# Kernel optimization log

Measured on AMD Instinct MI355X. Metric: run time of the kernel, lower is better.

Reference implementation:

```python
import jax, jax.numpy as jnp
import numpy as np

B, LQ, LK, H, A = 32, 2048, 2048, 1024, 512


def setup_inputs() -> dict:
    key = jax.random.key(0)
    ks = jax.random.split(key, 5)
    s = 1.0 / np.sqrt(H)
    return {
        "query": jax.random.normal(ks[0], (B, LQ, H), jnp.float32),
        "key": jax.random.normal(ks[1], (B, LK, H), jnp.float32),
        "Wq": jax.random.normal(ks[2], (H, A), jnp.float32) * s,
        "bq": jnp.zeros((A,), jnp.float32),
        "Wk": jax.random.normal(ks[3], (H, A), jnp.float32) * s,
        "bk": jnp.zeros((A,), jnp.float32),
        "Wv": jax.random.normal(ks[4], (A, 1), jnp.float32) * (1.0 / np.sqrt(A)),
        "bv": jnp.zeros((1,), jnp.float32),
    }


def reference(query, key, Wq, bq, Wk, bk, Wv, bv):
    # Linear projections
    Qp = jnp.einsum("bqh,ha->bqa", query, Wq) + bq          # [B, LQ, A]
    Kp = jnp.einsum("bkh,ha->bka", key, Wk) + bk            # [B, LK, A]
    # Score matrix Q(query) @ K(key)^T
    alpha_mat = jnp.einsum("bqa,bka->bqk", Qp, Kp)          # [B, LQ, LK]
    # Sum over query dim, softmax over key dim
    alpha = jax.nn.softmax(alpha_mat.sum(axis=1, keepdims=True), axis=2)  # [B, 1, LK]
    # Per-key scalar head V applied to projected keys, then weighted combine
    v = jnp.einsum("bka,ao->bko", Kp, Wv) + bv              # [B, LK, 1]
    x = jnp.matmul(alpha, v)[:, 0, :]                        # [B, 1]
    return x
```

## Files before the change

### kernel.cpp

```cpp
#include <hip/hip_runtime.h>
#include <math.h>

#define NB 32
#define LQ 2048
#define LK 2048
#define HD 1024
#define AD 512
#define QCH 32

__global__ void __launch_bounds__(256) k1_qreduce(const float* __restrict__ query,
                                                 const float* __restrict__ Wk,
                                                 const float* __restrict__ Wv,
                                                 const float* __restrict__ bk,
                                                 const float* __restrict__ bv,
                                                 float* __restrict__ partial,
                                                 float* __restrict__ wv_eff,
                                                 float* __restrict__ c_v) {
    int bid = blockIdx.x;
    if (bid < NB * QCH) {
        int b = bid / QCH, qc = bid % QCH;
        int t = threadIdx.x;
        const int QPC = LQ / QCH;
        float4 a0 = {0.f, 0.f, 0.f, 0.f};
        float4 a1 = {0.f, 0.f, 0.f, 0.f};
        const float4* src = (const float4*)(query + ((size_t)b * LQ + (size_t)qc * QPC) * HD);
        for (int q = 0; q < QPC; q += 2) {
            float4 v0 = src[(size_t)q * (HD / 4) + t];
            float4 v1 = src[(size_t)(q + 1) * (HD / 4) + t];
            a0.x += v0.x; a0.y += v0.y; a0.z += v0.z; a0.w += v0.w;
            a1.x += v1.x; a1.y += v1.y; a1.z += v1.z; a1.w += v1.w;
        }
        float4 acc = {a0.x + a1.x, a0.y + a1.y, a0.z + a1.z, a0.w + a1.w};
        float4* dst = (float4*)(partial + ((size_t)qc * NB + b) * HD);
        dst[t] = acc;
    } else if (bid < NB * QCH + 16) {
        int w = threadIdx.x >> 6, lane = threadIdx.x & 63;
        int gw = (bid - NB * QCH) * 4 + w;
        const float4* vv = (const float4*)(Wv);
        for (int r = 0; r < 16; ++r) {
            int h = gw * 16 + r;
            const float4* wr = (const float4*)(Wk + (size_t)h * AD);
            double acc = 0.0;
            #pragma unroll
            for (int j = 0; j < 2; ++j) {
                int f = lane + 64 * j;
                float4 w4 = wr[f];
                float4 v4 = vv[f];
                acc += (double)w4.x * (double)v4.x + (double)w4.y * (double)v4.y
                     + (double)w4.z * (double)v4.z + (double)w4.w * (double)v4.w;
            }
            #pragma unroll
            for (int off = 32; off > 0; off >>= 1) acc += __shfl_down(acc, off);
            if (lane == 0) wv_eff[h] = (float)acc;
        }
    } else {
        if (threadIdx.x < 64) {
            int lane = threadIdx.x;
            const float4* br = (const float4*)(bk);
            const float4* vv = (const float4*)(Wv);
            double acc = 0.0;
            #pragma unroll
            for (int j = 0; j < 2; ++j) {
                int f = lane + 64 * j;
                float4 b4 = br[f];
                float4 v4 = vv[f];
                acc += (double)b4.x * (double)v4.x + (double)b4.y * (double)v4.y
                     + (double)b4.z * (double)v4.z + (double)b4.w * (double)v4.w;
            }
            #pragma unroll
            for (int off = 32; off > 0; off >>= 1) acc += __shfl_down(acc, off);
            if (lane == 0) c_v[0] = (float)(acc + (double)bv[0]);
        }
    }
}

__global__ void __launch_bounds__(256) kB_qsum(const float* __restrict__ partial,
                                               const float* __restrict__ Wq,
                                               const float* __restrict__ bq,
                                               float* __restrict__ qsum) {
    __shared__ float sq[HD];
    __shared__ double red[4][64];
    int b = blockIdx.x >> 3;
    int a0 = (blockIdx.x & 7) * 64;
    int t = threadIdx.x;

    #pragma unroll
    for (int c = 0; c < 4; ++c) {
        int h = t + c * 256;
        float acc = 0.f;
        #pragma unroll 4
        for (int qc = 0; qc < QCH; ++qc)
            acc += partial[((size_t)qc * NB + b) * HD + h];
        sq[h] = acc;
    }
    __syncthreads();

    int w = t >> 6, lane = t & 63;
    int a = a0 + lane;
    const float* wp = Wq + a;
    double c0 = 0.0, c1 = 0.0, c2 = 0.0, c3 = 0.0;
    int hbase = w * 256;
    for (int i = 0; i < 256; i += 4) {
        int h = hbase + i;
        c0 += (double)sq[h]     * (double)wp[(size_t)h * AD];
        c1 += (double)sq[h + 1] * (double)wp[(size_t)(h + 1) * AD];
        c2 += (double)sq[h + 2] * (double)wp[(size_t)(h + 2) * AD];
        c3 += (double)sq[h + 3] * (double)wp[(size_t)(h + 3) * AD];
    }
    red[w][lane] = ((c0 + c1) + (c2 + c3));
    __syncthreads();
    if (t < 64) {
        double s = red[0][t] + red[1][t] + red[2][t] + red[3][t];
        qsum[(size_t)b * AD + a0 + t] = (float)(s + (double)LQ * (double)bq[a0 + t]);
    }
}

__global__ void __launch_bounds__(256) k4_weff(const float* __restrict__ qsum,
                                               const float* __restrict__ Wk,
                                               float* __restrict__ wk_eff) {
    int w = threadIdx.x >> 6, lane = threadIdx.x & 63;
    int widx = blockIdx.x * 4 + w;
    int b = widx >> 10, h = widx & (HD - 1);
    const float4* wr = (const float4*)(Wk + (size_t)h * AD);
    const float4* qs = (const float4*)(qsum + (size_t)b * AD);
    double acc = 0.0;
    #pragma unroll
    for (int j = 0; j < 2; ++j) {
        int f = lane + 64 * j;
        float4 w4 = wr[f];
        float4 q4 = qs[f];
        acc += (double)w4.x * (double)q4.x + (double)w4.y * (double)q4.y
             + (double)w4.z * (double)q4.z + (double)w4.w * (double)q4.w;
    }
    #pragma unroll
    for (int off = 32; off > 0; off >>= 1) acc += __shfl_down(acc, off);
    if (lane == 0) wk_eff[widx] = (float)acc;
}

__global__ void __launch_bounds__(256) k5_scores(const float* __restrict__ key,
                                                 const float* __restrict__ wk_eff,
                                                 const float* __restrict__ wv_eff,
                                                 const float* __restrict__ c_v,
                                                 float* __restrict__ scores,
                                                 float* __restrict__ vvals) {
    __shared__ float lwk[HD];
    __shared__ float lwv[HD];
    int bid = blockIdx.x;
    int b = bid >> 6;
    int k0 = (bid & 63) * 32;
    for (int i = threadIdx.x; i < HD; i += 256) {
        lwk[i] = wk_eff[(size_t)b * HD + i];
        lwv[i] = wv_eff[i];
    }
    __syncthreads();
    int w = threadIdx.x >> 6;
    int lane = threadIdx.x & 63;
    double cv = (double)c_v[0];
    const float4* lwk4 = (const float4*)lwk;
    const float4* lwv4 = (const float4*)lwv;
    for (int r = 0; r < 8; ++r) {
        int k = k0 + w * 8 + r;
        const float4* kr = (const float4*)(key + ((size_t)b * LK + k) * HD);
        double sc = 0.0, vv = 0.0;
        #pragma unroll
        for (int j = 0; j < 4; ++j) {
            int f = lane + 64 * j;
            float4 kv  = kr[f];
            float4 wk4 = lwk4[f];
            float4 wv4 = lwv4[f];
            sc += (double)kv.x * (double)wk4.x + (double)kv.y * (double)wk4.y
                + (double)kv.z * (double)wk4.z + (double)kv.w * (double)wk4.w;
            vv += (double)kv.x * (double)wv4.x + (double)kv.y * (double)wv4.y
                + (double)kv.z * (double)wv4.z + (double)kv.w * (double)wv4.w;
        }
        #pragma unroll
        for (int off = 32; off > 0; off >>= 1) {
            sc += __shfl_down(sc, off);
            vv += __shfl_down(vv, off);
        }
        if (lane == 0) {
            scores[(size_t)b * LK + k] = (float)sc;
            vvals[(size_t)b * LK + k]  = (float)(vv + cv);
        }
    }
}

__global__ void __launch_bounds__(256) k6_softmax(const float* __restrict__ scores,
                                                  const float* __restrict__ vvals,
                                                  float* __restrict__ out) {
    int b = blockIdx.x;
    int t = threadIdx.x;
    __shared__ float smax_sh[4];
    __shared__ double num_sh[4], den_sh[4];
    const float* sr = scores + (size_t)b * LK;
    const float* vr = vvals  + (size_t)b * LK;
    float m = -INFINITY;
    for (int k = t; k < LK; k += 256) m = fmaxf(m, sr[k]);
    #pragma unroll
    for (int off = 32; off > 0; off >>= 1) m = fmaxf(m, __shfl_down(m, off));
    int w = t >> 6, lane = t & 63;
    if (lane == 0) smax_sh[w] = m;
    __syncthreads();
    float gm = fmaxf(fmaxf(smax_sh[0], smax_sh[1]), fmaxf(smax_sh[2], smax_sh[3]));
    double num = 0.0, den = 0.0;
    for (int k = t; k < LK; k += 256) {
        double e = exp((double)(sr[k] - gm));
        den += e;
        num += e * (double)vr[k];
    }
    #pragma unroll
    for (int off = 32; off > 0; off >>= 1) {
        num += __shfl_down(num, off);
        den += __shfl_down(den, off);
    }
    if (lane == 0) { num_sh[w] = num; den_sh[w] = den; }
    __syncthreads();
    if (t == 0) {
        double N = num_sh[0] + num_sh[1] + num_sh[2] + num_sh[3];
        double D = den_sh[0] + den_sh[1] + den_sh[2] + den_sh[3];
        out[b] = (float)(N / D);
    }
}

extern "C" void kernel_launch(void* const* d_in, const int* in_sizes, int n_in,
                              void* d_out, int out_size, void* d_ws, size_t ws_size,
                              hipStream_t stream) {
    const float* query = (const float*)d_in[0];
    const float* key   = (const float*)d_in[1];
    const float* Wq    = (const float*)d_in[2];
    const float* bq    = (const float*)d_in[3];
    const float* Wk    = (const float*)d_in[4];
    const float* bk    = (const float*)d_in[5];
    const float* Wv    = (const float*)d_in[6];
    const float* bv    = (const float*)d_in[7];
    float* out = (float*)d_out;

    float* ws = (float*)d_ws;
    size_t off = 0;
    float* partial = ws + off; off += (size_t)QCH * NB * HD;
    float* qsum    = ws + off; off += (size_t)NB * AD;
    float* wk_eff  = ws + off; off += (size_t)NB * HD;
    float* wv_eff  = ws + off; off += (size_t)HD;
    float* c_v     = ws + off; off += 1;
    float* scores  = ws + off; off += (size_t)NB * LK;
    float* vvals   = ws + off; off += (size_t)NB * LK;

    hipLaunchKernelGGL(k1_qreduce, dim3(NB * QCH + 16 + 1), dim3(256), 0, stream,
                       query, Wk, Wv, bk, bv, partial, wv_eff, c_v);
    hipLaunchKernelGGL(kB_qsum, dim3(NB * 8), dim3(256), 0, stream, partial, Wq, bq, qsum);
    hipLaunchKernelGGL(k4_weff, dim3(NB * HD / 4), dim3(256), 0, stream, qsum, Wk, wk_eff);
    hipLaunchKernelGGL(k5_scores, dim3(NB * (LK / 32)), dim3(256), 0, stream,
                       key, wk_eff, wv_eff, c_v, scores, vvals);
    hipLaunchKernelGGL(k6_softmax, dim3(NB), dim3(256), 0, stream, scores, vvals, out);
}
```

Measured before the change: 148.6 us.

## Fuse all phases into one cooperative persistent kernel with grid syncs

Merges the five separate kernels into a single cooperative kernel that runs the phases in sequence, separated by grid-wide barriers, on a persistent grid sized by occupancy. It also regroups the work per block: phase 4 handles two key rows per iteration and phase 3 handles eight rows per wave. The goal is to remove per-kernel launch gaps and tail effects, at the cost of grid.sync overhead and a grid limited to resident blocks. A fallback path launches the phases as separate kernels if the cooperative launch fails.

```diff
diff --git a/kernel.cpp b/kernel.cpp
--- a/kernel.cpp
+++ b/kernel.cpp
@@ -1,5 +1,8 @@
 #include <hip/hip_runtime.h>
+#include <hip/hip_cooperative_groups.h>
 #include <math.h>
+
+namespace cg = cooperative_groups;
 
 #define NB 32
 #define LQ 2048
@@ -8,18 +11,10 @@
 #define AD 512
 #define QCH 32
 
-__global__ void __launch_bounds__(256) k1_qreduce(const float* __restrict__ query,
-                                                 const float* __restrict__ Wk,
-                                                 const float* __restrict__ Wv,
-                                                 const float* __restrict__ bk,
-                                                 const float* __restrict__ bv,
-                                                 float* __restrict__ partial,
-                                                 float* __restrict__ wv_eff,
-                                                 float* __restrict__ c_v) {
-    int bid = blockIdx.x;
-    if (bid < NB * QCH) {
-        int b = bid / QCH, qc = bid % QCH;
-        int t = threadIdx.x;
+__device__ __forceinline__ void phase1(int G, int bid, int t,
+        const float* __restrict__ query, float* __restrict__ partial) {
+    for (int task = bid; task < NB * QCH; task += G) {
+        int b = task / QCH, qc = task % QCH;
         const int QPC = LQ / QCH;
         float4 a0 = {0.f, 0.f, 0.f, 0.f};
         float4 a1 = {0.f, 0.f, 0.f, 0.f};
@@ -31,15 +26,55 @@
             a1.x += v1.x; a1.y += v1.y; a1.z += v1.z; a1.w += v1.w;
         }
         float4 acc = {a0.x + a1.x, a0.y + a1.y, a0.z + a1.z, a0.w + a1.w};
-        float4* dst = (float4*)(partial + ((size_t)qc * NB + b) * HD);
-        dst[t] = acc;
-    } else if (bid < NB * QCH + 16) {
-        int w = threadIdx.x >> 6, lane = threadIdx.x & 63;
-        int gw = (bid - NB * QCH) * 4 + w;
-        const float4* vv = (const float4*)(Wv);
-        for (int r = 0; r < 16; ++r) {
-            int h = gw * 16 + r;
+        ((float4*)(partial + ((size_t)qc * NB + b) * HD))[t] = acc;
+    }
+}
+
+__device__ __forceinline__ void phase2(int G, int bid, int t,
+        const float* __restrict__ partial, const float* __restrict__ Wq,
+        const float* __restrict__ bq, const float* __restrict__ Wk,
+        const float* __restrict__ Wv, const float* __restrict__ bk,
+        const float* __restrict__ bv, float* __restrict__ qsum,
+        float* __restrict__ wv_eff, float* __restrict__ c_v) {
+    __shared__ float sq[HD];
+    __shared__ double red[4][64];
+    int w = t >> 6, lane = t & 63;
+    for (int task = bid; task < 513; task += G) {
+        if (task < 256) {
+            int b = task >> 3;
+            int a0 = (task & 7) * 64;
+            #pragma unroll
+            for (int c = 0; c < 4; ++c) {
+                int h = t + c * 256;
+                float acc = 0.f;
+                #pragma unroll 4
+                for (int qc = 0; qc < QCH; ++qc)
+                    acc += partial[((size_t)qc * NB + b) * HD + h];
+                sq[h] = acc;
+            }
+            __syncthreads();
+            int a = a0 + lane;
+            const float* wp = Wq + a;
+            double c0 = 0.0, c1 = 0.0, c2 = 0.0, c3 = 0.0;
+            int hbase = w * 256;
+            for (int i = 0; i < 256; i += 4) {
+                int h = hbase + i;
+                c0 += (double)sq[h]     * (double)wp[(size_t)h * AD];
+                c1 += (double)sq[h + 1] * (double)wp[(size_t)(h + 1) * AD];
+                c2 += (double)sq[h + 2] * (double)wp[(size_t)(h + 2) * AD];
+                c3 += (double)sq[h + 3] * (double)wp[(size_t)(h + 3) * AD];
+            }
+            red[w][lane] = ((c0 + c1) + (c2 + c3));
+            __syncthreads();
+            if (t < 64) {
+                double s = red[0][t] + red[1][t] + red[2][t] + red[3][t];
+                qsum[(size_t)b * AD + a0 + t] = (float)(s + (double)LQ * (double)bq[a0 + t]);
+            }
+            __syncthreads();
+        } else if (task < 512) {
+            int h = (task - 256) * 4 + w;
             const float4* wr = (const float4*)(Wk + (size_t)h * AD);
+            const float4* vv = (const float4*)(Wv);
             double acc = 0.0;
             #pragma unroll
             for (int j = 0; j < 2; ++j) {
@@ -52,174 +87,205 @@
             #pragma unroll
             for (int off = 32; off > 0; off >>= 1) acc += __shfl_down(acc, off);
             if (lane == 0) wv_eff[h] = (float)acc;
-        }
-    } else {
-        if (threadIdx.x < 64) {
-            int lane = threadIdx.x;
-            const float4* br = (const float4*)(bk);
-            const float4* vv = (const float4*)(Wv);
+        } else {
+            if (t < 64) {
+                const float4* br = (const float4*)(bk);
+                const float4* vv = (const float4*)(Wv);
+                double acc = 0.0;
+                #pragma unroll
+                for (int j = 0; j < 2; ++j) {
+                    int f = lane + 64 * j;
+                    float4 b4 = br[f];
+                    float4 v4 = vv[f];
+                    acc += (double)b4.x * (double)v4.x + (double)b4.y * (double)v4.y
+                         + (double)b4.z * (double)v4.z + (double)b4.w * (double)v4.w;
+                }
+                #pragma unroll
+                for (int off = 32; off > 0; off >>= 1) acc += __shfl_down(acc, off);
+                if (lane == 0) c_v[0] = (float)(acc + (double)bv[0]);
+            }
+        }
+    }
+}
+
+__device__ __forceinline__ void phase3(int G, int bid, int t,
+        const float* __restrict__ qsum, const float* __restrict__ Wk,
+        float* __restrict__ wk_eff) {
+    int w = t >> 6, lane = t & 63;
+    for (int task = bid; task < 1024; task += G) {
+        int base = task * 32 + w * 8;
+        for (int r = 0; r < 8; ++r) {
+            int idx = base + r;
+            int b = idx >> 10, h = idx & (HD - 1);
+            const float4* wr = (const float4*)(Wk + (size_t)h * AD);
+            const float4* qs = (const float4*)(qsum + (size_t)b * AD);
             double acc = 0.0;
             #pragma unroll
             for (int j = 0; j < 2; ++j) {
                 int f = lane + 64 * j;
-                float4 b4 = br[f];
-                float4 v4 = vv[f];
-                acc += (double)b4.x * (double)v4.x + (double)b4.y * (double)v4.y
-                     + (double)b4.z * (double)v4.z + (double)b4.w * (double)v4.w;
+                float4 w4 = wr[f];
+                float4 q4 = qs[f];
+                acc += (double)w4.x * (double)q4.x + (double)w4.y * (double)q4.y
+                     + (double)w4.z * (double)q4.z + (double)w4.w * (double)q4.w;
             }
             #pragma unroll
             for (int off = 32; off > 0; off >>= 1) acc += __shfl_down(acc, off);
-            if (lane == 0) c_v[0] = (float)(acc + (double)bv[0]);
-        }
-    }
-}
-
-__global__ void __launch_bounds__(256) kB_qsum(const float* __restrict__ partial,
-                                               const float* __restrict__ Wq,
-                                               const float* __restrict__ bq,
-                                               float* __restrict__ qsum) {
-    __shared__ float sq[HD];
-    __shared__ double red[4][64];
-    int b = blockIdx.x >> 3;
-    int a0 = (blockIdx.x & 7) * 64;
-    int t = threadIdx.x;
-
-    #pragma unroll
-    for (int c = 0; c < 4; ++c) {
-        int h = t + c * 256;
-        float acc = 0.f;
-        #pragma unroll 4
-        for (int qc = 0; qc < QCH; ++qc)
-            acc += partial[((size_t)qc * NB + b) * HD + h];
-        sq[h] = acc;
-    }
-    __syncthreads();
-
-    int w = t >> 6, lane = t & 63;
-    int a = a0 + lane;
-    const float* wp = Wq + a;
-    double c0 = 0.0, c1 = 0.0, c2 = 0.0, c3 = 0.0;
-    int hbase = w * 256;
-    for (int i = 0; i < 256; i += 4) {
-        int h = hbase + i;
-        c0 += (double)sq[h]     * (double)wp[(size_t)h * AD];
-        c1 += (double)sq[h + 1] * (double)wp[(size_t)(h + 1) * AD];
-        c2 += (double)sq[h + 2] * (double)wp[(size_t)(h + 2) * AD];
-        c3 += (double)sq[h + 3] * (double)wp[(size_t)(h + 3) * AD];
-    }
-    red[w][lane] = ((c0 + c1) + (c2 + c3));
-    __syncthreads();
-    if (t < 64) {
-        double s = red[0][t] + red[1][t] + red[2][t] + red[3][t];
-        qsum[(size_t)b * AD + a0 + t] = (float)(s + (double)LQ * (double)bq[a0 + t]);
-    }
-}
-
-__global__ void __launch_bounds__(256) k4_weff(const float* __restrict__ qsum,
-                                               const float* __restrict__ Wk,
-                                               float* __restrict__ wk_eff) {
-    int w = threadIdx.x >> 6, lane = threadIdx.x & 63;
-    int widx = blockIdx.x * 4 + w;
-    int b = widx >> 10, h = widx & (HD - 1);
-    const float4* wr = (const float4*)(Wk + (size_t)h * AD);
-    const float4* qs = (const float4*)(qsum + (size_t)b * AD);
-    double acc = 0.0;
-    #pragma unroll
-    for (int j = 0; j < 2; ++j) {
-        int f = lane + 64 * j;
-        float4 w4 = wr[f];
-        float4 q4 = qs[f];
-        acc += (double)w4.x * (double)q4.x + (double)w4.y * (double)q4.y
-             + (double)w4.z * (double)q4.z + (double)w4.w * (double)q4.w;
-    }
-    #pragma unroll
-    for (int off = 32; off > 0; off >>= 1) acc += __shfl_down(acc, off);
-    if (lane == 0) wk_eff[widx] = (float)acc;
-}
-
-__global__ void __launch_bounds__(256) k5_scores(const float* __restrict__ key,
-                                                 const float* __restrict__ wk_eff,
-                                                 const float* __restrict__ wv_eff,
-                                                 const float* __restrict__ c_v,
-                                                 float* __restrict__ scores,
-                                                 float* __restrict__ vvals) {
+            if (lane == 0) wk_eff[idx] = (float)acc;
+        }
+    }
+}
+
+__device__ __forceinline__ void phase4(int G, int bid, int t,
+        const float* __restrict__ key, const float* __restrict__ wk_eff,
+        const float* __restrict__ wv_eff, const float* __restrict__ c_v,
+        float* __restrict__ scores, float* __restrict__ vvals) {
     __shared__ float lwk[HD];
     __shared__ float lwv[HD];
-    int bid = blockIdx.x;
-    int b = bid >> 6;
-    int k0 = (bid & 63) * 32;
-    for (int i = threadIdx.x; i < HD; i += 256) {
-        lwk[i] = wk_eff[(size_t)b * HD + i];
-        lwv[i] = wv_eff[i];
-    }
-    __syncthreads();
-    int w = threadIdx.x >> 6;
-    int lane = threadIdx.x & 63;
-    double cv = (double)c_v[0];
-    const float4* lwk4 = (const float4*)lwk;
-    const float4* lwv4 = (const float4*)lwv;
-    for (int r = 0; r < 8; ++r) {
-        int k = k0 + w * 8 + r;
-        const float4* kr = (const float4*)(key + ((size_t)b * LK + k) * HD);
-        double sc = 0.0, vv = 0.0;
+    int w = t >> 6, lane = t & 63;
+    for (int task = bid; task < 1024; task += G) {
+        int b = task >> 5;
+        int k0 = (task & 31) * 64;
+        for (int i = t; i < HD; i += 256) {
+            lwk[i] = wk_eff[(size_t)b * HD + i];
+            lwv[i] = wv_eff[i];
+        }
+        __syncthreads();
+        double cv = (double)c_v[0];
+        const float4* lwk4 = (const float4*)lwk;
+        const float4* lwv4 = (const float4*)lwv;
+        for (int rp = 0; rp < 8; ++rp) {
+            int k = k0 + w * 16 + rp * 2;
+            const float4* kr0 = (const float4*)(key + ((size_t)b * LK + k) * HD);
+            const float4* kr1 = kr0 + (HD / 4);
+            double sc0 = 0.0, vv0 = 0.0, sc1 = 0.0, vv1 = 0.0;
+            #pragma unroll
+            for (int j = 0; j < 4; ++j) {
+                int f = lane + 64 * j;
+                float4 k0v = kr0[f];
+                float4 k1v = kr1[f];
+                float4 wk4 = lwk4[f];
+                float4 wv4 = lwv4[f];
+                sc0 += (double)k0v.x * (double)wk4.x + (double)k0v.y * (double)wk4.y
+                     + (double)k0v.z * (double)wk4.z + (double)k0v.w * (double)wk4.w;
+                vv0 += (double)k0v.x * (double)wv4.x + (double)k0v.y * (double)wv4.y
+                     + (double)k0v.z * (double)wv4.z + (double)k0v.w * (double)wv4.w;
+                sc1 += (double)k1v.x * (double)wk4.x + (double)k1v.y * (double)wk4.y
+                     + (double)k1v.z * (double)wk4.z + (double)k1v.w * (double)wk4.w;
+                vv1 += (double)k1v.x * (double)wv4.x + (double)k1v.y * (double)wv4.y
+                     + (double)k1v.z * (double)wv4.z + (double)k1v.w * (double)wv4.w;
+            }
+            #pragma unroll
+            for (int off = 32; off > 0; off >>= 1) {
+                sc0 += __shfl_down(sc0, off);
+                vv0 += __shfl_down(vv0, off);
+                sc1 += __shfl_down(sc1, off);
+                vv1 += __shfl_down(vv1, off);
+            }
+            if (lane == 0) {
+                scores[(size_t)b * LK + k]     = (float)sc0;
+                vvals [(size_t)b * LK + k]     = (float)(vv0 + cv);
+                scores[(size_t)b * LK + k + 1] = (float)sc1;
+                vvals [(size_t)b * LK + k + 1] = (float)(vv1 + cv);
+            }
+        }
+        __syncthreads();
+    }
+}
+
+__device__ __forceinline__ void phase5(int G, int bid, int t,
+        const float* __restrict__ scores, const float* __restrict__ vvals,
+        float* __restrict__ out) {
+    __shared__ float smax_sh[4];
+    __shared__ double num_sh[4], den_sh[4];
+    int w = t >> 6, lane = t & 63;
+    for (int b = bid; b < NB; b += G) {
+        const float* sr = scores + (size_t)b * LK;
+        const float* vr = vvals  + (size_t)b * LK;
+        float m = -INFINITY;
+        for (int k = t; k < LK; k += 256) m = fmaxf(m, sr[k]);
         #pragma unroll
-        for (int j = 0; j < 4; ++j) {
-            int f = lane + 64 * j;
-            float4 kv  = kr[f];
-            float4 wk4 = lwk4[f];
-            float4 wv4 = lwv4[f];
-            sc += (double)kv.x * (double)wk4.x + (double)kv.y * (double)wk4.y
-                + (double)kv.z * (double)wk4.z + (double)kv.w * (double)wk4.w;
-            vv += (double)kv.x * (double)wv4.x + (double)kv.y * (double)wv4.y
-                + (double)kv.z * (double)wv4.z + (double)kv.w * (double)wv4.w;
+        for (int off = 32; off > 0; off >>= 1) m = fmaxf(m, __shfl_down(m, off));
+        if (lane == 0) smax_sh[w] = m;
+        __syncthreads();
+        float gm = fmaxf(fmaxf(smax_sh[0], smax_sh[1]), fmaxf(smax_sh[2], smax_sh[3]));
+        double num = 0.0, den = 0.0;
+        for (int k = t; k < LK; k += 256) {
+            double e = exp((double)(sr[k] - gm));
+            den += e;
+            num += e * (double)vr[k];
         }
         #pragma unroll
         for (int off = 32; off > 0; off >>= 1) {
-            sc += __shfl_down(sc, off);
-            vv += __shfl_down(vv, off);
-        }
-        if (lane == 0) {
-            scores[(size_t)b * LK + k] = (float)sc;
-            vvals[(size_t)b * LK + k]  = (float)(vv + cv);
-        }
-    }
-}
-
-__global__ void __launch_bounds__(256) k6_softmax(const float* __restrict__ scores,
-                                                  const float* __restrict__ vvals,
-                                                  float* __restrict__ out) {
-    int b = blockIdx.x;
-    int t = threadIdx.x;
-    __shared__ float smax_sh[4];
-    __shared__ double num_sh[4], den_sh[4];
-    const float* sr = scores + (size_t)b * LK;
-    const float* vr = vvals  + (size_t)b * LK;
-    float m = -INFINITY;
-    for (int k = t; k < LK; k += 256) m = fmaxf(m, sr[k]);
-    #pragma unroll
-    for (int off = 32; off > 0; off >>= 1) m = fmaxf(m, __shfl_down(m, off));
-    int w = t >> 6, lane = t & 63;
-    if (lane == 0) smax_sh[w] = m;
-    __syncthreads();
-    float gm = fmaxf(fmaxf(smax_sh[0], smax_sh[1]), fmaxf(smax_sh[2], smax_sh[3]));
-    double num = 0.0, den = 0.0;
-    for (int k = t; k < LK; k += 256) {
-        double e = exp((double)(sr[k] - gm));
-        den += e;
-        num += e * (double)vr[k];
-    }
-    #pragma unroll
-    for (int off = 32; off > 0; off >>= 1) {
-        num += __shfl_down(num, off);
-        den += __shfl_down(den, off);
-    }
-    if (lane == 0) { num_sh[w] = num; den_sh[w] = den; }
-    __syncthreads();
-    if (t == 0) {
-        double N = num_sh[0] + num_sh[1] + num_sh[2] + num_sh[3];
-        double D = den_sh[0] + den_sh[1] + den_sh[2] + den_sh[3];
-        out[b] = (float)(N / D);
-    }
+            num += __shfl_down(num, off);
+            den += __shfl_down(den, off);
+        }
+        if (lane == 0) { num_sh[w] = num; den_sh[w] = den; }
+        __syncthreads();
+        if (t == 0) {
+            double N = num_sh[0] + num_sh[1] + num_sh[2] + num_sh[3];
+            double D = den_sh[0] + den_sh[1] + den_sh[2] + den_sh[3];
+            out[b] = (float)(N / D);
+        }
+        __syncthreads();
+    }
+}
+
+__global__ void __launch_bounds__(256, 4)
+fused_all(const float* __restrict__ query, const float* __restrict__ key,
+          const float* __restrict__ Wq, const float* __restrict__ bq,
+          const float* __restrict__ Wk, const float* __restrict__ bk,
+          const float* __restrict__ Wv, const float* __restrict__ bv,
+          float* __restrict__ partial, float* __restrict__ qsum,
+          float* __restrict__ wk_eff, float* __restrict__ wv_eff,
+          float* __restrict__ c_v, float* __restrict__ scores,
+          float* __restrict__ vvals, float* __restrict__ out) {
+    cg::grid_group grid = cg::this_grid();
+    const int G = gridDim.x, bid = blockIdx.x, t = threadIdx.x;
+    phase1(G, bid, t, query, partial);
+    grid.sync();
+    phase2(G, bid, t, partial, Wq, bq, Wk, Wv, bk, bv, qsum, wv_eff, c_v);
+    grid.sync();
+    phase3(G, bid, t, qsum, Wk, wk_eff);
+    grid.sync();
+    phase4(G, bid, t, key, wk_eff, wv_eff, c_v, scores, vvals);
+    grid.sync();
+    phase5(G, bid, t, scores, vvals, out);
+}
+
+__global__ void __launch_bounds__(256) kp1(const float* __restrict__ query,
+                                           float* __restrict__ partial) {
+    phase1(gridDim.x, blockIdx.x, threadIdx.x, query, partial);
+}
+__global__ void __launch_bounds__(256) kp2(const float* __restrict__ partial,
+                                           const float* __restrict__ Wq,
+                                           const float* __restrict__ bq,
+                                           const float* __restrict__ Wk,
+                                           const float* __restrict__ Wv,
+                                           const float* __restrict__ bk,
+                                           const float* __restrict__ bv,
+                                           float* __restrict__ qsum,
+                                           float* __restrict__ wv_eff,
+                                           float* __restrict__ c_v) {
+    phase2(gridDim.x, blockIdx.x, threadIdx.x, partial, Wq, bq, Wk, Wv, bk, bv,
+           qsum, wv_eff, c_v);
+}
+__global__ void __launch_bounds__(256) kp3(const float* __restrict__ qsum,
+                                           const float* __restrict__ Wk,
+                                           float* __restrict__ wk_eff) {
+    phase3(gridDim.x, blockIdx.x, threadIdx.x, qsum, Wk, wk_eff);
+}
+__global__ void __launch_bounds__(256) kp4(const float* __restrict__ key,
+                                           const float* __restrict__ wk_eff,
+                                           const float* __restrict__ wv_eff,
+                                           const float* __restrict__ c_v,
+                                           float* __restrict__ scores,
+                                           float* __restrict__ vvals) {
+    phase4(gridDim.x, blockIdx.x, threadIdx.x, key, wk_eff, wv_eff, c_v, scores, vvals);
+}
+__global__ void __launch_bounds__(256) kp5(const float* __restrict__ scores,
+                                           const float* __restrict__ vvals,
+                                           float* __restrict__ out) {
+    phase5(gridDim.x, blockIdx.x, threadIdx.x, scores, vvals, out);
 }
 
 extern "C" void kernel_launch(void* const* d_in, const int* in_sizes, int n_in,
@@ -245,11 +311,37 @@
     float* scores  = ws + off; off += (size_t)NB * LK;
     float* vvals   = ws + off; off += (size_t)NB * LK;
 
-    hipLaunchKernelGGL(k1_qreduce, dim3(NB * QCH + 16 + 1), dim3(256), 0, stream,
-                       query, Wk, Wv, bk, bv, partial, wv_eff, c_v);
-    hipLaunchKernelGGL(kB_qsum, dim3(NB * 8), dim3(256), 0, stream, partial, Wq, bq, qsum);
-    hipLaunchKernelGGL(k4_weff, dim3(NB * HD / 4), dim3(256), 0, stream, qsum, Wk, wk_eff);
-    hipLaunchKernelGGL(k5_scores, dim3(NB * (LK / 32)), dim3(256), 0, stream,
-                       key, wk_eff, wv_eff, c_v, scores, vvals);
-    hipLaunchKernelGGL(k6_softmax, dim3(NB), dim3(256), 0, stream, scores, vvals, out);
-}
+    int dev = 0;
+    (void)hipGetDevice(&dev);
+    int numCU = 0;
+    (void)hipDeviceGetAttribute(&numCU, hipDeviceAttributeMultiprocessorCount, dev);
+    int maxBlk = 0;
+    hipError_t occ = hipOccupancyMaxActiveBlocksPerMultiprocessor(
+        &maxBlk, (const void*)fused_all, 256, 0);
+
+    hipError_t st = hipErrorUnknown;
+    if (occ == hipSuccess && numCU > 0 && maxBlk > 0) {
+        int G = maxBlk * numCU;
+        if (G > NB * QCH) G = NB * QCH;
+        if (G >= 64) {
+            void* args[] = {
+                (void*)&query, (void*)&key, (void*)&Wq, (void*)&bq,
+                (void*)&Wk, (void*)&bk, (void*)&Wv, (void*)&bv,
+                (void*)&partial, (void*)&qsum, (void*)&wk_eff, (void*)&wv_eff,
+                (void*)&c_v, (void*)&scores, (void*)&vvals, (void*)&out
+            };
+            st = hipLaunchCooperativeKernel((const void*)fused_all, dim3(G), dim3(256),
+                                            args, 0, stream);
+        }
+    }
+
+    if (st != hipSuccess) {
+        hipLaunchKernelGGL(kp1, dim3(NB * QCH), dim3(256), 0, stream, query, partial);
+        hipLaunchKernelGGL(kp2, dim3(513), dim3(256), 0, stream,
+                           partial, Wq, bq, Wk, Wv, bk, bv, qsum, wv_eff, c_v);
+        hipLaunchKernelGGL(kp3, dim3(1024), dim3(256), 0, stream, qsum, Wk, wk_eff);
+        hipLaunchKernelGGL(kp4, dim3(1024), dim3(256), 0, stream,
+                           key, wk_eff, wv_eff, c_v, scores, vvals);
+        hipLaunchKernelGGL(kp5, dim3(NB), dim3(256), 0, stream, scores, vvals, out);
+    }
+}
```

Measured after the change: 395.9 us. 2.66x slower.

## Precompute Wk·Wq^T product, merge reduction kernels, fuse softmax via last-block atomic

Applied to the files above, without the earlier changes.

The query-side chain is reassociated. A 1024x1024 matrix MT = Wk·Wq^T is built with an LDS-tiled fp32 GEMM inside the first kernel, alongside the query row-sum blocks. wk_eff is then one matvec of the summed query against MT plus a bias term, which removes the separate qsum and weff kernels. The softmax-weighted combine moves into the score kernel: the last block per batch, found with an atomic counter, does the final reduction. This cuts launches from five to three, but adds a roughly 1G-FLOP weight GEMM per call and a workspace-size fallback path.

```diff
diff --git a/kernel.cpp b/kernel.cpp
--- a/kernel.cpp
+++ b/kernel.cpp
@@ -8,18 +8,21 @@
 #define AD 512
 #define QCH 32
 
-__global__ void __launch_bounds__(256) k1_qreduce(const float* __restrict__ query,
-                                                 const float* __restrict__ Wk,
-                                                 const float* __restrict__ Wv,
-                                                 const float* __restrict__ bk,
-                                                 const float* __restrict__ bv,
-                                                 float* __restrict__ partial,
-                                                 float* __restrict__ wv_eff,
-                                                 float* __restrict__ c_v) {
-    int bid = blockIdx.x;
-    if (bid < NB * QCH) {
-        int b = bid / QCH, qc = bid % QCH;
-        int t = threadIdx.x;
+__global__ void __launch_bounds__(256, 4)
+k1_main(const float* __restrict__ query, const float* __restrict__ Wq,
+        const float* __restrict__ Wk, const float* __restrict__ Wv,
+        const float* __restrict__ bq, const float* __restrict__ bk,
+        const float* __restrict__ bv, float* __restrict__ partial,
+        float* __restrict__ MT, float* __restrict__ wv_eff,
+        float* __restrict__ ck, float* __restrict__ c_v) {
+    __shared__ float wq_l[128][33];
+    __shared__ float wk_l[32][33];
+    const int bid = blockIdx.x;
+    const int t = threadIdx.x;
+
+    if (bid >= 256) {
+        int task = bid - 256;
+        int b = task / QCH, qc = task % QCH;
         const int QPC = LQ / QCH;
         float4 a0 = {0.f, 0.f, 0.f, 0.f};
         float4 a1 = {0.f, 0.f, 0.f, 0.f};
@@ -31,12 +34,251 @@
             a1.x += v1.x; a1.y += v1.y; a1.z += v1.z; a1.w += v1.w;
         }
         float4 acc = {a0.x + a1.x, a0.y + a1.y, a0.z + a1.z, a0.w + a1.w};
-        float4* dst = (float4*)(partial + ((size_t)qc * NB + b) * HD);
-        dst[t] = acc;
+        ((float4*)(partial + ((size_t)qc * NB + b) * HD))[t] = acc;
+        return;
+    }
+
+    const int hb = bid >> 3;
+    const int pb = bid & 7;
+    const int hgrp = t >> 5;
+    const int pgrp = t & 31;
+    float acc[4][4] = {{0.f}};
+    for (int ac = 0; ac < 16; ++ac) {
+        for (int s = t; s < 128 * 32; s += 256) {
+            int row = s >> 5, a = s & 31;
+            wq_l[row][a] = Wq[(size_t)(pb * 128 + row) * AD + ac * 32 + a];
+        }
+        for (int s = t; s < 32 * 32; s += 256) {
+            int row = s >> 5, a = s & 31;
+            wk_l[row][a] = Wk[(size_t)(hb * 32 + row) * AD + ac * 32 + a];
+        }
+        __syncthreads();
+        #pragma unroll 8
+        for (int a = 0; a < 32; ++a) {
+            float k0 = wk_l[hgrp][a],      k1 = wk_l[hgrp + 8][a],
+                  k2 = wk_l[hgrp + 16][a], k3 = wk_l[hgrp + 24][a];
+            float q0 = wq_l[pgrp][a],      q1 = wq_l[pgrp + 32][a],
+                  q2 = wq_l[pgrp + 64][a], q3 = wq_l[pgrp + 96][a];
+            acc[0][0] += k0*q0; acc[0][1] += k0*q1; acc[0][2] += k0*q2; acc[0][3] += k0*q3;
+            acc[1][0] += k1*q0; acc[1][1] += k1*q1; acc[1][2] += k1*q2; acc[1][3] += k1*q3;
+            acc[2][0] += k2*q0; acc[2][1] += k2*q1; acc[2][2] += k2*q2; acc[2][3] += k2*q3;
+            acc[3][0] += k3*q0; acc[3][1] += k3*q1; acc[3][2] += k3*q2; acc[3][3] += k3*q3;
+        }
+        __syncthreads();
+    }
+    #pragma unroll
+    for (int i = 0; i < 4; ++i)
+        #pragma unroll
+        for (int j = 0; j < 4; ++j)
+            MT[(size_t)(hb * 32 + hgrp + 8 * i) * HD + pb * 128 + pgrp + 32 * j] = acc[i][j];
+
+    if (pb == 0) {
+        int w = t >> 6, lane = t & 63;
+        const float4* vv4 = (const float4*)Wv;
+        const float4* bq4 = (const float4*)bq;
+        for (int rr = 0; rr < 8; ++rr) {
+            int h = hb * 32 + w * 8 + rr;
+            const float4* wr = (const float4*)(Wk + (size_t)h * AD);
+            double a1 = 0.0, a2 = 0.0;
+            #pragma unroll
+            for (int j = 0; j < 2; ++j) {
+                int f = lane + 64 * j;
+                float4 w4 = wr[f];
+                float4 v4 = vv4[f];
+                float4 b4 = bq4[f];
+                a1 += (double)w4.x * v4.x + (double)w4.y * v4.y
+                    + (double)w4.z * v4.z + (double)w4.w * v4.w;
+                a2 += (double)b4.x * w4.x + (double)b4.y * w4.y
+                    + (double)b4.z * w4.z + (double)b4.w * w4.w;
+            }
+            #pragma unroll
+            for (int off = 32; off > 0; off >>= 1) {
+                a1 += __shfl_down(a1, off);
+                a2 += __shfl_down(a2, off);
+            }
+            if (lane == 0) {
+                wv_eff[h] = (float)a1;
+                ck[h] = (float)((double)LQ * a2);
+            }
+        }
+    }
+    if (bid == 0 && t < 64) {
+        int lane = t;
+        const float4* br = (const float4*)bk;
+        const float4* vv4 = (const float4*)Wv;
+        double acc2 = 0.0;
+        #pragma unroll
+        for (int j = 0; j < 2; ++j) {
+            int f = lane + 64 * j;
+            float4 b4 = br[f];
+            float4 v4 = vv4[f];
+            acc2 += (double)b4.x * v4.x + (double)b4.y * v4.y
+                  + (double)b4.z * v4.z + (double)b4.w * v4.w;
+        }
+        #pragma unroll
+        for (int off = 32; off > 0; off >>= 1) acc2 += __shfl_down(acc2, off);
+        if (lane == 0) c_v[0] = (float)(acc2 + (double)bv[0]);
+    }
+}
+
+__global__ void __launch_bounds__(256)
+k2_wkeff(const float* __restrict__ partial, const float* __restrict__ MT,
+         const float* __restrict__ ck, float* __restrict__ wk_eff,
+         int* __restrict__ cnt) {
+    __shared__ float sq[HD];
+    const int bid = blockIdx.x;
+    const int t = threadIdx.x;
+    const int b = bid >> 3, hc = bid & 7;
+    if (bid == 0 && t < NB) cnt[t] = 0;
+    for (int h = t; h < HD; h += 256) {
+        float acc = 0.f;
+        #pragma unroll 4
+        for (int qc = 0; qc < QCH; ++qc)
+            acc += partial[((size_t)qc * NB + b) * HD + h];
+        sq[h] = acc;
+    }
+    __syncthreads();
+    int w = t >> 6, lane = t & 63;
+    const float4* sq4 = (const float4*)sq;
+    for (int rr = 0; rr < 32; ++rr) {
+        int h = hc * 128 + w * 32 + rr;
+        const float4* m4 = (const float4*)(MT + (size_t)h * HD);
+        double acc = 0.0;
+        #pragma unroll
+        for (int f0 = 0; f0 < 4; ++f0) {
+            int f = lane + 64 * f0;
+            float4 m = m4[f];
+            float4 s = sq4[f];
+            acc += (double)m.x * s.x + (double)m.y * s.y
+                 + (double)m.z * s.z + (double)m.w * s.w;
+        }
+        #pragma unroll
+        for (int off = 32; off > 0; off >>= 1) acc += __shfl_down(acc, off);
+        if (lane == 0) wk_eff[(size_t)b * HD + h] = (float)(acc + (double)ck[h]);
+    }
+}
+
+__global__ void __launch_bounds__(256)
+k3_scores(const float* __restrict__ key, const float* __restrict__ wk_eff,
+          const float* __restrict__ wv_eff, const float* __restrict__ c_v,
+          float* __restrict__ scores, float* __restrict__ vvals,
+          int* __restrict__ cnt, float* __restrict__ out) {
+    __shared__ float lwk[HD];
+    __shared__ float lwv[HD];
+    __shared__ int lastFlag;
+    __shared__ float smax_sh[4];
+    __shared__ double num_sh[4], den_sh[4];
+    const int bid = blockIdx.x;
+    const int b = bid >> 6;
+    const int k0 = (bid & 63) * 32;
+    const int t = threadIdx.x;
+    for (int i = t; i < HD; i += 256) {
+        lwk[i] = wk_eff[(size_t)b * HD + i];
+        lwv[i] = wv_eff[i];
+    }
+    __syncthreads();
+    int w = t >> 6, lane = t & 63;
+    double cv = (double)c_v[0];
+    const float4* lwk4 = (const float4*)lwk;
+    const float4* lwv4 = (const float4*)lwv;
+    for (int rp = 0; rp < 4; ++rp) {
+        int k = k0 + w * 8 + rp * 2;
+        const float4* kr0 = (const float4*)(key + ((size_t)b * LK + k) * HD);
+        const float4* kr1 = kr0 + (HD / 4);
+        double sc0 = 0.0, vv0 = 0.0, sc1 = 0.0, vv1 = 0.0;
+        #pragma unroll
+        for (int j = 0; j < 4; ++j) {
+            int f = lane + 64 * j;
+            float4 k0v = kr0[f];
+            float4 k1v = kr1[f];
+            float4 wk4 = lwk4[f];
+            float4 wv4 = lwv4[f];
+            sc0 += (double)k0v.x * wk4.x + (double)k0v.y * wk4.y
+                 + (double)k0v.z * wk4.z + (double)k0v.w * wk4.w;
+            vv0 += (double)k0v.x * wv4.x + (double)k0v.y * wv4.y
+                 + (double)k0v.z * wv4.z + (double)k0v.w * wv4.w;
+            sc1 += (double)k1v.x * wk4.x + (double)k1v.y * wk4.y
+                 + (double)k1v.z * wk4.z + (double)k1v.w * wk4.w;
+            vv1 += (double)k1v.x * wv4.x + (double)k1v.y * wv4.y
+                 + (double)k1v.z * wv4.z + (double)k1v.w * wv4.w;
+        }
+        #pragma unroll
+        for (int off = 32; off > 0; off >>= 1) {
+            sc0 += __shfl_down(sc0, off);
+            vv0 += __shfl_down(vv0, off);
+            sc1 += __shfl_down(sc1, off);
+            vv1 += __shfl_down(vv1, off);
+        }
+        if (lane == 0) {
+            scores[(size_t)b * LK + k]     = (float)sc0;
+            vvals [(size_t)b * LK + k]     = (float)(vv0 + cv);
+            scores[(size_t)b * LK + k + 1] = (float)sc1;
+            vvals [(size_t)b * LK + k + 1] = (float)(vv1 + cv);
+        }
+    }
+    __syncthreads();
+    if (t == 0) {
+        __threadfence();
+        int old = atomicAdd(&cnt[b], 1);
+        lastFlag = (old == 63) ? 1 : 0;
+    }
+    __syncthreads();
+    if (!lastFlag) return;
+    __threadfence();
+
+    const float* sr = scores + (size_t)b * LK;
+    const float* vr = vvals  + (size_t)b * LK;
+    float m = -INFINITY;
+    for (int k = t; k < LK; k += 256) m = fmaxf(m, sr[k]);
+    #pragma unroll
+    for (int off = 32; off > 0; off >>= 1) m = fmaxf(m, __shfl_down(m, off));
+    if (lane == 0) smax_sh[w] = m;
+    __syncthreads();
+    float gm = fmaxf(fmaxf(smax_sh[0], smax_sh[1]), fmaxf(smax_sh[2], smax_sh[3]));
+    double num = 0.0, den = 0.0;
+    for (int k = t; k < LK; k += 256) {
+        double e = exp((double)(sr[k] - gm));
+        den += e;
+        num += e * (double)vr[k];
+    }
+    #pragma unroll
+    for (int off = 32; off > 0; off >>= 1) {
+        num += __shfl_down(num, off);
+        den += __shfl_down(den, off);
+    }
+    if (lane == 0) { num_sh[w] = num; den_sh[w] = den; }
+    __syncthreads();
+    if (t == 0) {
+        double N = num_sh[0] + num_sh[1] + num_sh[2] + num_sh[3];
+        double D = den_sh[0] + den_sh[1] + den_sh[2] + den_sh[3];
+        out[b] = (float)(N / D);
+    }
+}
+
+__global__ void __launch_bounds__(256)
+fbA(const float* __restrict__ query, const float* __restrict__ Wk,
+    const float* __restrict__ Wv, const float* __restrict__ bk,
+    const float* __restrict__ bv, float* __restrict__ partial,
+    float* __restrict__ wv_eff, float* __restrict__ c_v) {
+    int bid = blockIdx.x;
+    int t = threadIdx.x;
+    if (bid < NB * QCH) {
+        int b = bid / QCH, qc = bid % QCH;
+        const int QPC = LQ / QCH;
+        float4 a0 = {0.f,0.f,0.f,0.f}, a1 = {0.f,0.f,0.f,0.f};
+        const float4* src = (const float4*)(query + ((size_t)b * LQ + (size_t)qc * QPC) * HD);
+        for (int q = 0; q < QPC; q += 2) {
+            float4 v0 = src[(size_t)q * (HD / 4) + t];
+            float4 v1 = src[(size_t)(q + 1) * (HD / 4) + t];
+            a0.x += v0.x; a0.y += v0.y; a0.z += v0.z; a0.w += v0.w;
+            a1.x += v1.x; a1.y += v1.y; a1.z += v1.z; a1.w += v1.w;
+        }
+        float4 acc = {a0.x + a1.x, a0.y + a1.y, a0.z + a1.z, a0.w + a1.w};
+        ((float4*)(partial + ((size_t)qc * NB + b) * HD))[t] = acc;
     } else if (bid < NB * QCH + 16) {
-        int w = threadIdx.x >> 6, lane = threadIdx.x & 63;
+        int w = t >> 6, lane = t & 63;
         int gw = (bid - NB * QCH) * 4 + w;
-        const float4* vv = (const float4*)(Wv);
+        const float4* vv = (const float4*)Wv;
         for (int r = 0; r < 16; ++r) {
             int h = gw * 16 + r;
             const float4* wr = (const float4*)(Wk + (size_t)h * AD);
@@ -46,44 +288,41 @@
                 int f = lane + 64 * j;
                 float4 w4 = wr[f];
                 float4 v4 = vv[f];
-                acc += (double)w4.x * (double)v4.x + (double)w4.y * (double)v4.y
-                     + (double)w4.z * (double)v4.z + (double)w4.w * (double)v4.w;
+                acc += (double)w4.x * v4.x + (double)w4.y * v4.y
+                     + (double)w4.z * v4.z + (double)w4.w * v4.w;
             }
             #pragma unroll
             for (int off = 32; off > 0; off >>= 1) acc += __shfl_down(acc, off);
             if (lane == 0) wv_eff[h] = (float)acc;
         }
-    } else {
-        if (threadIdx.x < 64) {
-            int lane = threadIdx.x;
-            const float4* br = (const float4*)(bk);
-            const float4* vv = (const float4*)(Wv);
-            double acc = 0.0;
-            #pragma unroll
-            for (int j = 0; j < 2; ++j) {
-                int f = lane + 64 * j;
-                float4 b4 = br[f];
-                float4 v4 = vv[f];
-                acc += (double)b4.x * (double)v4.x + (double)b4.y * (double)v4.y
-                     + (double)b4.z * (double)v4.z + (double)b4.w * (double)v4.w;
-            }
-            #pragma unroll
-            for (int off = 32; off > 0; off >>= 1) acc += __shfl_down(acc, off);
-            if (lane == 0) c_v[0] = (float)(acc + (double)bv[0]);
-        }
-    }
-}
-
-__global__ void __launch_bounds__(256) kB_qsum(const float* __restrict__ partial,
-                                               const float* __restrict__ Wq,
-                                               const float* __restrict__ bq,
-                                               float* __restrict__ qsum) {
+    } else if (t < 64) {
+        int lane = t;
+        const float4* br = (const float4*)bk;
+        const float4* vv = (const float4*)Wv;
+        double acc = 0.0;
+        #pragma unroll
+        for (int j = 0; j < 2; ++j) {
+            int f = lane + 64 * j;
+            float4 b4 = br[f];
+            float4 v4 = vv[f];
+            acc += (double)b4.x * v4.x + (double)b4.y * v4.y
+                 + (double)b4.z * v4.z + (double)b4.w * v4.w;
+        }
+        #pragma unroll
+        for (int off = 32; off > 0; off >>= 1) acc += __shfl_down(acc, off);
+        if (lane == 0) c_v[0] = (float)(acc + (double)bv[0]);
+    }
+}
+
+__global__ void __launch_bounds__(256)
+fbB(const float* __restrict__ partial, const float* __restrict__ Wq,
+    const float* __restrict__ bq, float* __restrict__ qsum, int* __restrict__ cnt) {
     __shared__ float sq[HD];
     __shared__ double red[4][64];
     int b = blockIdx.x >> 3;
     int a0 = (blockIdx.x & 7) * 64;
     int t = threadIdx.x;
-
+    if (blockIdx.x == 0 && t < NB) cnt[t] = 0;
     #pragma unroll
     for (int c = 0; c < 4; ++c) {
         int h = t + c * 256;
@@ -94,7 +333,6 @@
         sq[h] = acc;
     }
     __syncthreads();
-
     int w = t >> 6, lane = t & 63;
     int a = a0 + lane;
     const float* wp = Wq + a;
@@ -102,22 +340,22 @@
     int hbase = w * 256;
     for (int i = 0; i < 256; i += 4) {
         int h = hbase + i;
-        c0 += (double)sq[h]     * (double)wp[(size_t)h * AD];
-        c1 += (double)sq[h + 1] * (double)wp[(size_t)(h + 1) * AD];
-        c2 += (double)sq[h + 2] * (double)wp[(size_t)(h + 2) * AD];
-        c3 += (double)sq[h + 3] * (double)wp[(size_t)(h + 3) * AD];
+        c0 += (double)sq[h]     * wp[(size_t)h * AD];
+        c1 += (double)sq[h + 1] * wp[(size_t)(h + 1) * AD];
+        c2 += (double)sq[h + 2] * wp[(size_t)(h + 2) * AD];
+        c3 += (double)sq[h + 3] * wp[(size_t)(h + 3) * AD];
     }
     red[w][lane] = ((c0 + c1) + (c2 + c3));
     __syncthreads();
     if (t < 64) {
         double s = red[0][t] + red[1][t] + red[2][t] + red[3][t];
-        qsum[(size_t)b * AD + a0 + t] = (float)(s + (double)LQ * (double)bq[a0 + t]);
-    }
-}
-
-__global__ void __launch_bounds__(256) k4_weff(const float* __restrict__ qsum,
-                                               const float* __restrict__ Wk,
-                                               float* __restrict__ wk_eff) {
+        qsum[(size_t)b * AD + a0 + t] = (float)(s + (double)LQ * bq[a0 + t]);
+    }
+}
+
+__global__ void __launch_bounds__(256)
+fbC(const float* __restrict__ qsum, const float* __restrict__ Wk,
+    float* __restrict__ wk_eff) {
     int w = threadIdx.x >> 6, lane = threadIdx.x & 63;
     int widx = blockIdx.x * 4 + w;
     int b = widx >> 10, h = widx & (HD - 1);
@@ -129,97 +367,12 @@
         int f = lane + 64 * j;
         float4 w4 = wr[f];
         float4 q4 = qs[f];
-        acc += (double)w4.x * (double)q4.x + (double)w4.y * (double)q4.y
-             + (double)w4.z * (double)q4.z + (double)w4.w * (double)q4.w;
+        acc += (double)w4.x * q4.x + (double)w4.y * q4.y
+             + (double)w4.z * q4.z + (double)w4.w * q4.w;
     }
     #pragma unroll
     for (int off = 32; off > 0; off >>= 1) acc += __shfl_down(acc, off);
     if (lane == 0) wk_eff[widx] = (float)acc;
-}
-
-__global__ void __launch_bounds__(256) k5_scores(const float* __restrict__ key,
-                                                 const float* __restrict__ wk_eff,
-                                                 const float* __restrict__ wv_eff,
-                                                 const float* __restrict__ c_v,
-                                                 float* __restrict__ scores,
-                                                 float* __restrict__ vvals) {
-    __shared__ float lwk[HD];
-    __shared__ float lwv[HD];
-    int bid = blockIdx.x;
-    int b = bid >> 6;
-    int k0 = (bid & 63) * 32;
-    for (int i = threadIdx.x; i < HD; i += 256) {
-        lwk[i] = wk_eff[(size_t)b * HD + i];
-        lwv[i] = wv_eff[i];
-    }
-    __syncthreads();
-    int w = threadIdx.x >> 6;
-    int lane = threadIdx.x & 63;
-    double cv = (double)c_v[0];
-    const float4* lwk4 = (const float4*)lwk;
-    const float4* lwv4 = (const float4*)lwv;
-    for (int r = 0; r < 8; ++r) {
-        int k = k0 + w * 8 + r;
-        const float4* kr = (const float4*)(key + ((size_t)b * LK + k) * HD);
-        double sc = 0.0, vv = 0.0;
-        #pragma unroll
-        for (int j = 0; j < 4; ++j) {
-            int f = lane + 64 * j;
-            float4 kv  = kr[f];
-            float4 wk4 = lwk4[f];
-            float4 wv4 = lwv4[f];
-            sc += (double)kv.x * (double)wk4.x + (double)kv.y * (double)wk4.y
-                + (double)kv.z * (double)wk4.z + (double)kv.w * (double)wk4.w;
-            vv += (double)kv.x * (double)wv4.x + (double)kv.y * (double)wv4.y
-                + (double)kv.z * (double)wv4.z + (double)kv.w * (double)wv4.w;
-        }
-        #pragma unroll
-        for (int off = 32; off > 0; off >>= 1) {
-            sc += __shfl_down(sc, off);
-            vv += __shfl_down(vv, off);
-        }
-        if (lane == 0) {
-            scores[(size_t)b * LK + k] = (float)sc;
-            vvals[(size_t)b * LK + k]  = (float)(vv + cv);
-        }
-    }
-}
-
-__global__ void __launch_bounds__(256) k6_softmax(const float* __restrict__ scores,
-                                                  const float* __restrict__ vvals,
-                                                  float* __restrict__ out) {
-    int b = blockIdx.x;
-    int t = threadIdx.x;
-    __shared__ float smax_sh[4];
-    __shared__ double num_sh[4], den_sh[4];
-    const float* sr = scores + (size_t)b * LK;
-    const float* vr = vvals  + (size_t)b * LK;
-    float m = -INFINITY;
-    for (int k = t; k < LK; k += 256) m = fmaxf(m, sr[k]);
-    #pragma unroll
-    for (int off = 32; off > 0; off >>= 1) m = fmaxf(m, __shfl_down(m, off));
-    int w = t >> 6, lane = t & 63;
-    if (lane == 0) smax_sh[w] = m;
-    __syncthreads();
-    float gm = fmaxf(fmaxf(smax_sh[0], smax_sh[1]), fmaxf(smax_sh[2], smax_sh[3]));
-    double num = 0.0, den = 0.0;
-    for (int k = t; k < LK; k += 256) {
-        double e = exp((double)(sr[k] - gm));
-        den += e;
-        num += e * (double)vr[k];
-    }
-    #pragma unroll
-    for (int off = 32; off > 0; off >>= 1) {
-        num += __shfl_down(num, off);
-        den += __shfl_down(den, off);
-    }
-    if (lane == 0) { num_sh[w] = num; den_sh[w] = den; }
-    __syncthreads();
-    if (t == 0) {
-        double N = num_sh[0] + num_sh[1] + num_sh[2] + num_sh[3];
-        double D = den_sh[0] + den_sh[1] + den_sh[2] + den_sh[3];
-        out[b] = (float)(N / D);
-    }
 }
 
 extern "C" void kernel_launch(void* const* d_in, const int* in_sizes, int n_in,
@@ -238,18 +391,33 @@
     float* ws = (float*)d_ws;
     size_t off = 0;
     float* partial = ws + off; off += (size_t)QCH * NB * HD;
-    float* qsum    = ws + off; off += (size_t)NB * AD;
+    float* MT      = ws + off; off += (size_t)HD * HD;
     float* wk_eff  = ws + off; off += (size_t)NB * HD;
     float* wv_eff  = ws + off; off += (size_t)HD;
+    float* ck      = ws + off; off += (size_t)HD;
     float* c_v     = ws + off; off += 1;
     float* scores  = ws + off; off += (size_t)NB * LK;
     float* vvals   = ws + off; off += (size_t)NB * LK;
-
-    hipLaunchKernelGGL(k1_qreduce, dim3(NB * QCH + 16 + 1), dim3(256), 0, stream,
-                       query, Wk, Wv, bk, bv, partial, wv_eff, c_v);
-    hipLaunchKernelGGL(kB_qsum, dim3(NB * 8), dim3(256), 0, stream, partial, Wq, bq, qsum);
-    hipLaunchKernelGGL(k4_weff, dim3(NB * HD / 4), dim3(256), 0, stream, qsum, Wk, wk_eff);
-    hipLaunchKernelGGL(k5_scores, dim3(NB * (LK / 32)), dim3(256), 0, stream,
-                       key, wk_eff, wv_eff, c_v, scores, vvals);
-    hipLaunchKernelGGL(k6_softmax, dim3(NB), dim3(256), 0, stream, scores, vvals, out);
-}
+    int*   cnt     = (int*)(ws + off); off += NB;
+    size_t need_main = off * sizeof(float);
+
+    if (ws_size >= need_main) {
+        hipLaunchKernelGGL(k1_main, dim3(256 + NB * QCH), dim3(256), 0, stream,
+                           query, Wq, Wk, Wv, bq, bk, bv,
+                           partial, MT, wv_eff, ck, c_v);
+        hipLaunchKernelGGL(k2_wkeff, dim3(256), dim3(256), 0, stream,
+                           partial, MT, ck, wk_eff, cnt);
+        hipLaunchKernelGGL(k3_scores, dim3(NB * (LK / 32)), dim3(256), 0, stream,
+                           key, wk_eff, wv_eff, c_v, scores, vvals, cnt, out);
+    } else {
+        float* qsum = MT;
+        hipLaunchKernelGGL(fbA, dim3(NB * QCH + 16 + 1), dim3(256), 0, stream,
+                           query, Wk, Wv, bk, bv, partial, wv_eff, c_v);
+        hipLaunchKernelGGL(fbB, dim3(256), dim3(256), 0, stream,
+                           partial, Wq, bq, qsum, cnt);
+        hipLaunchKernelGGL(fbC, dim3(NB * HD / 4), dim3(256), 0, stream,
+                           qsum, Wk, wk_eff);
+        hipLaunchKernelGGL(k3_scores, dim3(NB * (LK / 32)), dim3(256), 0, stream,
+                           key, wk_eff, wv_eff, c_v, scores, vvals, cnt, out);
+    }
+}
```

Result: slower. 329.8 us (+121.9%).
